# Kernel optimization log

Measured on AMD Instinct MI355X. Metric: run time of the kernel, lower is better.

The kernel has to match this reference:

```python
import jax, jax.numpy as jnp
import numpy as np

N_NODES = 100000
N_EDGES = 2400000


def setup_inputs() -> dict:
    key = jax.random.key(0)
    ks = jax.random.split(key, 6)
    x = jax.random.normal(ks[0], (N_NODES, 2), dtype=jnp.float32)
    edge_index = jax.random.randint(ks[1], (2, N_EDGES), 0, N_NODES, dtype=jnp.int64)
    # GCNConv weights (glorot-ish scale) and zero biases
    W1 = jax.random.normal(ks[2], (2, 32), dtype=jnp.float32) * (1.0 / np.sqrt(2.0))
    b1 = jnp.zeros((32,), dtype=jnp.float32)
    W2 = jax.random.normal(ks[3], (32, 32), dtype=jnp.float32) * (1.0 / np.sqrt(32.0))
    b2 = jnp.zeros((32,), dtype=jnp.float32)
    W3 = jax.random.normal(ks[4], (32, 1), dtype=jnp.float32) * (1.0 / np.sqrt(32.0))
    b3 = jnp.zeros((1,), dtype=jnp.float32)
    return {"x": x, "edge_index": edge_index, "W1": W1, "b1": b1,
            "W2": W2, "b2": b2, "W3": W3, "b3": b3}


def reference(x, edge_index, W1, b1, W2, b2, W3, b3):
    N = x.shape[0]
    self_loops = jnp.arange(N, dtype=edge_index.dtype)
    src = jnp.concatenate([edge_index[0], self_loops])  # message sources
    dst = jnp.concatenate([edge_index[1], self_loops])  # aggregation targets
    # Symmetric GCN normalization: deg computed at target nodes (PyG gcn_norm)
    deg = jax.ops.segment_sum(jnp.ones_like(dst, dtype=x.dtype), dst, num_segments=N)
    dinv = jnp.where(deg > 0, jax.lax.rsqrt(deg), 0.0)
    norm = (dinv[src] * dinv[dst])[:, None]  # [E+N, 1]

    def gcn_layer(h, W, b):
        h = h @ W                                  # [N, out]
        msg = norm * h[src]                        # gather + scale
        agg = jax.ops.segment_sum(msg, dst, num_segments=N)  # scatter-add
        return agg + b

    h = jax.nn.relu(gcn_layer(x, W1, b1))
    h = jax.nn.relu(gcn_layer(h, W2, b2))
    out = gcn_layer(h, W3, b3)
    return out.reshape(-1)
```

## Files before the change

### kernel.cpp

```cpp
#include <hip/hip_runtime.h>

#define NN 100000
#define NE 2400000
#define NB 391
#define CAP 6912

__device__ __forceinline__ int wexscan(int v, int lane) {
    int x = v;
#pragma unroll
    for (int off = 1; off < 64; off <<= 1) {
        int t = __shfl_up(x, off, 64);
        x += (lane >= off) ? t : 0;
    }
    return x - v;
}

__global__ __launch_bounds__(512) void k_binscatter(const int* __restrict__ ei,
        int* __restrict__ cur, int* __restrict__ binned) {
    __shared__ int hist[NB], lbase[NB], myb[NB];
    __shared__ int stage[4096];
    __shared__ unsigned short stageb[4096];
    __shared__ int wsum[8];
    int tid = threadIdx.x;
    for (int i = tid; i < NB; i += 512) hist[i] = 0;
    __syncthreads();
    int base_e = blockIdx.x * 4096 + tid * 8;
    int pk[8], bn[8], rk[8];
    if (base_e + 8 <= NE) {
        const int4* s4 = (const int4*)(ei + base_e);
        const int4* d4 = (const int4*)(ei + NE + base_e);
        int4 sa = s4[0], sb = s4[1], da = d4[0], db = d4[1];
        int ss[8] = {sa.x, sa.y, sa.z, sa.w, sb.x, sb.y, sb.z, sb.w};
        int dd[8] = {da.x, da.y, da.z, da.w, db.x, db.y, db.z, db.w};
#pragma unroll
        for (int k = 0; k < 8; ++k) {
            bn[k] = dd[k] >> 8;
            pk[k] = ss[k] | ((dd[k] & 255) << 17);
            rk[k] = atomicAdd(&hist[bn[k]], 1);
        }
    } else {
#pragma unroll
        for (int k = 0; k < 8; ++k) bn[k] = -1;
    }
    __syncthreads();
    int lane = tid & 63, wid = tid >> 6;
    int v = (tid < NB) ? hist[tid] : 0;
    int ex = wexscan(v, lane);
    if (lane == 63) wsum[wid] = ex + v;
    __syncthreads();
    int woff = 0, tot = 0;
#pragma unroll
    for (int i = 0; i < 8; ++i) {
        int s = wsum[i];
        woff += (i < wid) ? s : 0;
        tot += s;
    }
    ex += woff;
    if (tid < NB) {
        lbase[tid] = ex;
        if (v > 0) myb[tid] = tid * CAP + atomicAdd(&cur[tid], v);
    }
    __syncthreads();
#pragma unroll
    for (int k = 0; k < 8; ++k) {
        if (bn[k] >= 0) {
            int slot = lbase[bn[k]] + rk[k];
            stage[slot] = pk[k];
            stageb[slot] = (unsigned short)bn[k];
        }
    }
    __syncthreads();
    for (int j = tid; j < tot; j += 512) {
        int b = stageb[j];
        binned[myb[b] + (j - lbase[b])] = stage[j];
    }
}

__global__ __launch_bounds__(256) void k_csr_count(const int* __restrict__ binned,
        const int* __restrict__ cur, const float* __restrict__ x,
        int* __restrict__ rsp, float* __restrict__ dinv, float2* __restrict__ xs) {
    __shared__ int cnt[256];
    __shared__ int wsum[4];
    int tid = threadIdx.x, b = blockIdx.x;
    int base = b * CAP, n = cur[b];
    cnt[tid] = 0;
    __syncthreads();
    int n4 = n >> 2;
    const int4* b4 = (const int4*)(binned + base);
    for (int j = tid; j < n4; j += 256) {
        int4 w = b4[j];
        atomicAdd(&cnt[(w.x >> 17) & 255], 1);
        atomicAdd(&cnt[(w.y >> 17) & 255], 1);
        atomicAdd(&cnt[(w.z >> 17) & 255], 1);
        atomicAdd(&cnt[(w.w >> 17) & 255], 1);
    }
    for (int j = (n4 << 2) + tid; j < n; j += 256)
        atomicAdd(&cnt[(binned[base + j] >> 17) & 255], 1);
    __syncthreads();
    int deg = cnt[tid];
    int lane = tid & 63, wid = tid >> 6;
    int ex = wexscan(deg, lane);
    if (lane == 63) wsum[wid] = ex + deg;
    __syncthreads();
    int woff = 0;
#pragma unroll
    for (int i = 0; i < 4; ++i) woff += (i < wid) ? wsum[i] : 0;
    ex += woff;
    int node = (b << 8) + tid;
    if (node < NN) {
        rsp[node] = ((base + ex) << 8) | deg;
        float di = rsqrtf((float)(deg + 1));
        dinv[node] = di;
        float2 xv = ((const float2*)x)[node];
        xs[node] = make_float2(di * xv.x, di * xv.y);
    }
}

__global__ __launch_bounds__(256) void k_csr_place(const int* __restrict__ binned,
        const int* __restrict__ cur, const int* __restrict__ rsp,
        const float2* __restrict__ xs, const float* __restrict__ dinv,
        int* __restrict__ csr, float4* __restrict__ At) {
    __shared__ int cur2[256];
    int tid = threadIdx.x, b = blockIdx.x;
    int base = b * CAP, n = cur[b];
    int node = (b << 8) + tid;
    int rp = (node < NN) ? rsp[node] : 0;
    cur2[tid] = (node < NN) ? ((rp >> 8) - base) : 0;
    __syncthreads();
    int n4 = n >> 2;
    const int4* b4 = (const int4*)(binned + base);
    for (int j = tid; j < n4; j += 256) {
        int4 w = b4[j];
        int p0 = atomicAdd(&cur2[(w.x >> 17) & 255], 1); csr[base + p0] = w.x & 0x1FFFF;
        int p1 = atomicAdd(&cur2[(w.y >> 17) & 255], 1); csr[base + p1] = w.y & 0x1FFFF;
        int p2 = atomicAdd(&cur2[(w.z >> 17) & 255], 1); csr[base + p2] = w.z & 0x1FFFF;
        int p3 = atomicAdd(&cur2[(w.w >> 17) & 255], 1); csr[base + p3] = w.w & 0x1FFFF;
    }
    for (int j = (n4 << 2) + tid; j < n; j += 256) {
        int w = binned[base + j];
        int p = atomicAdd(&cur2[(w >> 17) & 255], 1);
        csr[base + p] = w & 0x1FFFF;
    }
    __syncthreads();
    if (node < NN) {
        int beg = rp >> 8, deg = rp & 255;
        float ax = 0.f, ay = 0.f;
        int e = beg, end = beg + deg;
        for (; e + 4 <= end; e += 4) {
            int s0 = csr[e], s1 = csr[e + 1], s2 = csr[e + 2], s3 = csr[e + 3];
            float2 v0 = xs[s0], v1 = xs[s1], v2 = xs[s2], v3 = xs[s3];
            ax += (v0.x + v1.x) + (v2.x + v3.x);
            ay += (v0.y + v1.y) + (v2.y + v3.y);
        }
        for (; e < end; ++e) { float2 vv = xs[csr[e]]; ax += vv.x; ay += vv.y; }
        float di = dinv[node];
        float2 xn = xs[node];
        At[node] = make_float4(di * (ax + xn.x), di * (ay + xn.y), di, 0.f);
    }
}

__global__ __launch_bounds__(256) void k_gather_fly(const float4* __restrict__ At,
        const int* __restrict__ rsp, const int* __restrict__ csr,
        const float* __restrict__ W1, const float* __restrict__ b1,
        const float* __restrict__ W2, const float* __restrict__ b2,
        const float* __restrict__ W3, float* __restrict__ h3) {
    __shared__ float Ws[1024];
    __shared__ float accS[256];
    __shared__ float4 stage[8][32];
    int tid = threadIdx.x;
    for (int j = tid; j < 1024; j += 256) Ws[j] = W2[j];
    int g = tid >> 5, f = tid & 31;
    int node = blockIdx.x * 8 + g;
    float w0f = W1[f], w1f = W1[32 + f], bf = b1[f];
    float4 an = At[node];
    int r = rsp[node];
    float di = an.z;
    float vs = fmaf(an.y, w1f, fmaf(an.x, w0f, bf));
    float acc0 = di * fmaxf(vs, 0.f), acc1 = 0.f;
    int beg = r >> 8, deg = r & 255;
    float4* st = &stage[g][0];
    for (int b0 = 0; b0 < deg; b0 += 32) {
        float4 a = make_float4(0.f, 0.f, 0.f, 0.f);
        if (b0 + f < deg) a = At[csr[beg + b0 + f]];
        st[f] = a;
        __asm__ __volatile__("" ::: "memory");
#pragma unroll
        for (int j = 0; j < 32; j += 2) {
            float4 e0 = st[j], e1 = st[j + 1];
            float v0 = fmaf(e0.y, w1f, fmaf(e0.x, w0f, bf));
            acc0 = fmaf(e0.z, fmaxf(v0, 0.f), acc0);
            float v1 = fmaf(e1.y, w1f, fmaf(e1.x, w0f, bf));
            acc1 = fmaf(e1.z, fmaxf(v1, 0.f), acc1);
        }
        __asm__ __volatile__("" ::: "memory");
    }
    accS[tid] = di * (acc0 + acc1);
    __syncthreads();
    int n0 = tid & 224;
    float sum = b2[f];
#pragma unroll
    for (int k = 0; k < 32; ++k) sum = fmaf(accS[n0 + k], Ws[(k << 5) + f], sum);
    float h2 = fmaxf(sum, 0.f);
    float v = di * h2 * W3[f];
#pragma unroll
    for (int off = 16; off > 0; off >>= 1) v += __shfl_down(v, off, 32);
    if (f == 0) h3[node] = v;
}

__global__ __launch_bounds__(256) void k_gather_out(const float* __restrict__ hs,
        const int* __restrict__ rsp, const int* __restrict__ csr,
        const float* __restrict__ dinv, const float* __restrict__ bias,
        float* __restrict__ out) {
    int node = blockIdx.x * 256 + threadIdx.x;
    if (node >= NN) return;
    int r = rsp[node];
    int beg = r >> 8, end = beg + (r & 255);
    float acc = hs[node];
    int e = beg;
    for (; e + 4 <= end; e += 4) {
        int s0 = csr[e], s1 = csr[e + 1], s2 = csr[e + 2], s3 = csr[e + 3];
        acc += (hs[s0] + hs[s1]) + (hs[s2] + hs[s3]);
    }
    for (; e < end; ++e) acc += hs[csr[e]];
    out[node] = dinv[node] * acc + bias[0];
}

extern "C" void kernel_launch(void* const* d_in, const int* in_sizes, int n_in,
                              void* d_out, int out_size, void* d_ws, size_t ws_size,
                              hipStream_t stream) {
    const float* x  = (const float*)d_in[0];
    const int*   ei = (const int*)d_in[1];
    const float* W1 = (const float*)d_in[2];
    const float* b1 = (const float*)d_in[3];
    const float* W2 = (const float*)d_in[4];
    const float* b2 = (const float*)d_in[5];
    const float* W3 = (const float*)d_in[6];
    const float* b3 = (const float*)d_in[7];
    float* out = (float*)d_out;

    char* w = (char*)d_ws;
    float4* At    = (float4*)w; w += NN * 16;
    float2* xs    = (float2*)w; w += NN * 8;
    int*   cur    = (int*)w;    w += NB * 4;
    int*   rsp    = (int*)w;    w += NN * 4;
    float* dinv   = (float*)w;  w += NN * 4;
    int*   binned = (int*)w;    w += NB * CAP * 4;
    int*   csr    = (int*)w;    w += NB * CAP * 4;
    float* h3     = (float*)w;  w += NN * 4;

    const int G_E4K = (NE + 4095) / 4096;
    const int G_N   = (NN + 255) / 256;
    const int G_G   = NN / 8;

    hipMemsetAsync(cur, 0, NB * 4, stream);
    k_binscatter<<<G_E4K, 512, 0, stream>>>(ei, cur, binned);
    k_csr_count<<<NB, 256, 0, stream>>>(binned, cur, x, rsp, dinv, xs);
    k_csr_place<<<NB, 256, 0, stream>>>(binned, cur, rsp, xs, dinv, csr, At);
    k_gather_fly<<<G_G, 256, 0, stream>>>(At, rsp, csr, W1, b1, W2, b2, W3, h3);
    k_gather_out<<<G_N, 256, 0, stream>>>(h3, rsp, csr, dinv, b3, out);
}
```

Measured before the change: 190.5 us.

## Merge CSR count and place into one kernel, split layer-1 aggregation out, transpose W2

The degree count/prefix scan and the CSR placement now run in a single per-bin kernel that reuses the in-block exclusive scan as the placement cursor. This drops a launch and the re-read of rsp. The layer-1 aggregation of xs moves into a separate per-node kernel, which is needed because xs must be complete across all bins before any node gathers from it. Separately, W2 is stored transposed and padded in shared memory so the dense 32x32 step can use float4 LDS reads for both operands.

```diff
diff --git a/kernel.cpp b/kernel.cpp
--- a/kernel.cpp
+++ b/kernel.cpp
@@ -76,10 +76,11 @@
     }
 }
 
-__global__ __launch_bounds__(256) void k_csr_count(const int* __restrict__ binned,
+__global__ __launch_bounds__(256) void k_build(const int* __restrict__ binned,
         const int* __restrict__ cur, const float* __restrict__ x,
-        int* __restrict__ rsp, float* __restrict__ dinv, float2* __restrict__ xs) {
-    __shared__ int cnt[256];
+        int* __restrict__ rsp, float* __restrict__ dinv, float2* __restrict__ xs,
+        int* __restrict__ csr) {
+    __shared__ int cnt[256], cur2[256];
     __shared__ int wsum[4];
     int tid = threadIdx.x, b = blockIdx.x;
     int base = b * CAP, n = cur[b];
@@ -114,21 +115,8 @@
         float2 xv = ((const float2*)x)[node];
         xs[node] = make_float2(di * xv.x, di * xv.y);
     }
-}
-
-__global__ __launch_bounds__(256) void k_csr_place(const int* __restrict__ binned,
-        const int* __restrict__ cur, const int* __restrict__ rsp,
-        const float2* __restrict__ xs, const float* __restrict__ dinv,
-        int* __restrict__ csr, float4* __restrict__ At) {
-    __shared__ int cur2[256];
-    int tid = threadIdx.x, b = blockIdx.x;
-    int base = b * CAP, n = cur[b];
-    int node = (b << 8) + tid;
-    int rp = (node < NN) ? rsp[node] : 0;
-    cur2[tid] = (node < NN) ? ((rp >> 8) - base) : 0;
-    __syncthreads();
-    int n4 = n >> 2;
-    const int4* b4 = (const int4*)(binned + base);
+    cur2[tid] = ex;
+    __syncthreads();
     for (int j = tid; j < n4; j += 256) {
         int4 w = b4[j];
         int p0 = atomicAdd(&cur2[(w.x >> 17) & 255], 1); csr[base + p0] = w.x & 0x1FFFF;
@@ -141,22 +129,27 @@
         int p = atomicAdd(&cur2[(w >> 17) & 255], 1);
         csr[base + p] = w & 0x1FFFF;
     }
-    __syncthreads();
-    if (node < NN) {
-        int beg = rp >> 8, deg = rp & 255;
-        float ax = 0.f, ay = 0.f;
-        int e = beg, end = beg + deg;
-        for (; e + 4 <= end; e += 4) {
-            int s0 = csr[e], s1 = csr[e + 1], s2 = csr[e + 2], s3 = csr[e + 3];
-            float2 v0 = xs[s0], v1 = xs[s1], v2 = xs[s2], v3 = xs[s3];
-            ax += (v0.x + v1.x) + (v2.x + v3.x);
-            ay += (v0.y + v1.y) + (v2.y + v3.y);
-        }
-        for (; e < end; ++e) { float2 vv = xs[csr[e]]; ax += vv.x; ay += vv.y; }
-        float di = dinv[node];
-        float2 xn = xs[node];
-        At[node] = make_float4(di * (ax + xn.x), di * (ay + xn.y), di, 0.f);
-    }
+}
+
+__global__ __launch_bounds__(256) void k_at(const int* __restrict__ rsp,
+        const int* __restrict__ csr, const float2* __restrict__ xs,
+        const float* __restrict__ dinv, float4* __restrict__ At) {
+    int node = blockIdx.x * 256 + threadIdx.x;
+    if (node >= NN) return;
+    int r = rsp[node];
+    int beg = r >> 8, end = beg + (r & 255);
+    float ax = 0.f, ay = 0.f;
+    int e = beg;
+    for (; e + 4 <= end; e += 4) {
+        int s0 = csr[e], s1 = csr[e + 1], s2 = csr[e + 2], s3 = csr[e + 3];
+        float2 v0 = xs[s0], v1 = xs[s1], v2 = xs[s2], v3 = xs[s3];
+        ax += (v0.x + v1.x) + (v2.x + v3.x);
+        ay += (v0.y + v1.y) + (v2.y + v3.y);
+    }
+    for (; e < end; ++e) { float2 vv = xs[csr[e]]; ax += vv.x; ay += vv.y; }
+    float di = dinv[node];
+    float2 xn = xs[node];
+    At[node] = make_float4(di * (ax + xn.x), di * (ay + xn.y), di, 0.f);
 }
 
 __global__ __launch_bounds__(256) void k_gather_fly(const float4* __restrict__ At,
@@ -164,11 +157,14 @@
         const float* __restrict__ W1, const float* __restrict__ b1,
         const float* __restrict__ W2, const float* __restrict__ b2,
         const float* __restrict__ W3, float* __restrict__ h3) {
-    __shared__ float Ws[1024];
+    __shared__ float WsT[32 * 36];
     __shared__ float accS[256];
     __shared__ float4 stage[8][32];
     int tid = threadIdx.x;
-    for (int j = tid; j < 1024; j += 256) Ws[j] = W2[j];
+    for (int j = tid; j < 1024; j += 256) {
+        int k = j >> 5, fo = j & 31;
+        WsT[fo * 36 + k] = W2[j];
+    }
     int g = tid >> 5, f = tid & 31;
     int node = blockIdx.x * 8 + g;
     float w0f = W1[f], w1f = W1[32 + f], bf = b1[f];
@@ -198,8 +194,16 @@
     __syncthreads();
     int n0 = tid & 224;
     float sum = b2[f];
-#pragma unroll
-    for (int k = 0; k < 32; ++k) sum = fmaf(accS[n0 + k], Ws[(k << 5) + f], sum);
+    const float* wrow = &WsT[f * 36];
+#pragma unroll
+    for (int k = 0; k < 32; k += 4) {
+        float4 a4 = *(const float4*)&accS[n0 + k];
+        float4 w4 = *(const float4*)&wrow[k];
+        sum = fmaf(a4.x, w4.x, sum);
+        sum = fmaf(a4.y, w4.y, sum);
+        sum = fmaf(a4.z, w4.z, sum);
+        sum = fmaf(a4.w, w4.w, sum);
+    }
     float h2 = fmaxf(sum, 0.f);
     float v = di * h2 * W3[f];
 #pragma unroll
@@ -254,8 +258,8 @@
 
     hipMemsetAsync(cur, 0, NB * 4, stream);
     k_binscatter<<<G_E4K, 512, 0, stream>>>(ei, cur, binned);
-    k_csr_count<<<NB, 256, 0, stream>>>(binned, cur, x, rsp, dinv, xs);
-    k_csr_place<<<NB, 256, 0, stream>>>(binned, cur, rsp, xs, dinv, csr, At);
+    k_build<<<NB, 256, 0, stream>>>(binned, cur, x, rsp, dinv, xs, csr);
+    k_at<<<G_N, 256, 0, stream>>>(rsp, csr, xs, dinv, At);
     k_gather_fly<<<G_G, 256, 0, stream>>>(At, rsp, csr, W1, b1, W2, b2, W3, h3);
     k_gather_out<<<G_N, 256, 0, stream>>>(h3, rsp, csr, dinv, b3, out);
 }
```

Result: slower. 195.2 us (+2.5%).
